# Kernel tuning notes

Measured on AMD Instinct MI355X. Metric: run time of the kernel, lower is better.

Reference implementation:

```python
import jax, jax.numpy as jnp
import numpy as np

N_NODES = 100000
N_EDGES = 1600000
D = 128
HID = 256  # min(2*D, 256)
D_OUT = 128
BN_EPS = 1e-5


def setup_inputs() -> dict:
    key = jax.random.key(0)
    ks = jax.random.split(key, 16)
    s = 0.05
    inp = {
        "x": jax.random.normal(ks[0], (N_NODES, D), dtype=jnp.float32),
        "edges": jax.random.randint(ks[1], (2, N_EDGES), 0, N_NODES, dtype=jnp.int32),
        # affine_before_rnn: Linear(D, D)
        "W_aff": jax.random.normal(ks[2], (D, D), dtype=jnp.float32) * s,
        "b_aff": jnp.zeros((D,), dtype=jnp.float32),
        # GRUCell(D, D)
        "W_ih": jax.random.normal(ks[3], (3 * D, D), dtype=jnp.float32) * s,
        "b_ih": jnp.zeros((3 * D,), dtype=jnp.float32),
        "W_hh": jax.random.normal(ks[4], (3 * D, D), dtype=jnp.float32) * s,
        "b_hh": jnp.zeros((3 * D,), dtype=jnp.float32),
        # merge_layer: Linear(2*D, D)
        "W_merge": jax.random.normal(ks[5], (D, 2 * D), dtype=jnp.float32) * s,
        "b_merge": jnp.zeros((D,), dtype=jnp.float32),
        # learnable self-connection weight
        "eps": jnp.asarray(1.0, dtype=jnp.float32),
        # backbone: Linear(D, HID) -> relu -> Linear(HID, D_OUT) -> relu -> BatchNorm1d
        "W1": jax.random.normal(ks[6], (HID, D), dtype=jnp.float32) * s,
        "b1": jnp.zeros((HID,), dtype=jnp.float32),
        "W2": jax.random.normal(ks[7], (D_OUT, HID), dtype=jnp.float32) * s,
        "b2": jnp.zeros((D_OUT,), dtype=jnp.float32),
        "gamma": jnp.ones((D_OUT,), dtype=jnp.float32),
        "beta": jnp.zeros((D_OUT,), dtype=jnp.float32),
    }
    return inp


def reference(x, edges, W_aff, b_aff, W_ih, b_ih, W_hh, b_hh,
              W_merge, b_merge, eps, W1, b1, W2, b2, gamma, beta):
    src, dst = edges[0], edges[1]
    n = x.shape[0]

    # ---- aggregation 1: 'sum' -> scatter-sum of neighbor features ----
    agg_sum = jax.ops.segment_sum(x[src], dst, num_segments=n)  # (N, D)

    # ---- aggregation 2: 'rnn-max' -> affine, scatter-max, GRUCell ----
    xi = x @ W_aff.T + b_aff
    agg_max = jax.ops.segment_max(xi[src], dst, num_segments=n)  # (N, D)
    agg_max = jnp.where(jnp.isfinite(agg_max), agg_max, 0.0)  # empty segments -> 0

    # GRUCell: input = aggregated neighbors, hidden = original node features
    gi = agg_max @ W_ih.T + b_ih  # (N, 3D)
    gh = x @ W_hh.T + b_hh        # (N, 3D)
    ir, iz, inn = jnp.split(gi, 3, axis=1)
    hr, hz, hn = jnp.split(gh, 3, axis=1)
    r = jax.nn.sigmoid(ir + hr)
    z = jax.nn.sigmoid(iz + hz)
    ncand = jnp.tanh(inn + r * hn)
    rnn_out = (1.0 - z) * ncand + z * x  # (N, D)

    # ---- merge ('cat') ----
    h = jnp.concatenate([agg_sum, rnn_out], axis=1) @ W_merge.T + b_merge  # (N, D)

    # ---- learnable self-connection ----
    h = h + eps * x

    # ---- backbone: dense -> relu -> dense -> relu -> batchnorm1d (train mode) ----
    h = jax.nn.relu(h @ W1.T + b1)
    h = jax.nn.relu(h @ W2.T + b2)
    mean = jnp.mean(h, axis=0)
    var = jnp.mean(jnp.square(h - mean), axis=0)  # biased batch variance
    out = gamma * (h - mean) * jax.lax.rsqrt(var + BN_EPS) + beta
    return out
```

## Files before the change

### kernel.cpp

```cpp
#include <hip/hip_runtime.h>
#include <hip/hip_bf16.h>
#include <math.h>

using bf16 = __hip_bfloat16;
typedef __attribute__((ext_vector_type(8))) short bf16x8;
typedef __attribute__((ext_vector_type(4))) float f32x4;

__device__ __forceinline__ float b2f(unsigned short u) {
  return __uint_as_float(((unsigned)u) << 16);
}
__device__ __forceinline__ unsigned short f2b(float f) {
  bf16 h = __float2bfloat16(f);
  return *reinterpret_cast<unsigned short*>(&h);
}
__device__ __forceinline__ ushort4 f2b4(float4 v) {
  return make_ushort4(f2b(v.x), f2b(v.y), f2b(v.z), f2b(v.w));
}

__global__ __launch_bounds__(256) void mgemm_k(
    const unsigned short* __restrict__ A, int lda, const float* __restrict__ W,
    const float* __restrict__ bias, unsigned short* __restrict__ Cb, int ldc,
    int N, int M, int K) {
  constexpr int LDA = 72;
  __shared__ unsigned short As[128 * LDA];
  __shared__ unsigned short Ws[128 * LDA];

  const int tid = threadIdx.x;
  const int lane = tid & 63;
  const int wave = tid >> 6;
  const int row0 = blockIdx.y * 128;
  const int m0 = blockIdx.x * 128;
  const int rowhalf = (wave & 1) * 64;
  const int colhalf = (wave >> 1) * 64;
  const int l15 = lane & 15;
  const int quad = lane >> 4;

  f32x4 acc[4][4] = {};

  for (int kc = 0; kc < K; kc += 64) {
#pragma unroll
    for (int i = 0; i < 4; i++) {
      int idx = tid + i * 256;
      int r = idx >> 3;
      int k8 = (idx & 7) * 8;
      int row = row0 + r;
      ushort4 u0 = make_ushort4(0, 0, 0, 0), u1 = u0;
      if (row < N) {
        const unsigned short* s = A + (size_t)row * lda + kc + k8;
        u0 = *(const ushort4*)s;
        u1 = *(const ushort4*)(s + 4);
      }
      *(ushort4*)&As[r * LDA + k8] = u0;
      *(ushort4*)&As[r * LDA + k8 + 4] = u1;
    }
#pragma unroll
    for (int i = 0; i < 8; i++) {
      int idx = tid + i * 256;
      int r = idx >> 4;
      int k4 = idx & 15;
      float4 v = *(const float4*)(W + (size_t)(m0 + r) * K + kc + k4 * 4);
      *(ushort4*)&Ws[r * LDA + k4 * 4] = f2b4(v);
    }
    __syncthreads();
#pragma unroll
    for (int ks = 0; ks < 2; ks++) {
      const int ko = ks * 32 + quad * 8;
      bf16x8 af[4], wf[4];
#pragma unroll
      for (int ri = 0; ri < 4; ri++)
        af[ri] = *(const bf16x8*)&As[(rowhalf + ri * 16 + l15) * LDA + ko];
#pragma unroll
      for (int ci = 0; ci < 4; ci++)
        wf[ci] = *(const bf16x8*)&Ws[(colhalf + ci * 16 + l15) * LDA + ko];
#pragma unroll
      for (int ri = 0; ri < 4; ri++)
#pragma unroll
        for (int ci = 0; ci < 4; ci++)
          acc[ri][ci] = __builtin_amdgcn_mfma_f32_16x16x32_bf16(
              af[ri], wf[ci], acc[ri][ci], 0, 0, 0);
    }
    __syncthreads();
  }
#pragma unroll
  for (int ci = 0; ci < 4; ci++) {
    const int col = m0 + colhalf + ci * 16 + l15;
    const float bv = bias[col];
#pragma unroll
    for (int ri = 0; ri < 4; ri++) {
      const int rbase = row0 + rowhalf + ri * 16 + quad * 4;
#pragma unroll
      for (int r = 0; r < 4; r++) {
        int row = rbase + r;
        if (row >= N) continue;
        Cb[(size_t)row * ldc + col] = f2b(acc[ri][ci][r] + bv);
      }
    }
  }
}

__global__ __launch_bounds__(256) void grurnn_k(
    const unsigned short* __restrict__ aggm,
    const unsigned short* __restrict__ xcat,
    const unsigned short* __restrict__ Wbig,
    const float* __restrict__ bias_big, unsigned short* __restrict__ Bcat,
    int N) {
  constexpr int LDA = 72;
  __shared__ unsigned short As[32 * LDA];

  const int tid = threadIdx.x;
  const int lane = tid & 63;
  const int wave = tid >> 6;
  const int l15 = lane & 15;
  const int quad = lane >> 4;
  const int row0 = blockIdx.x * 32;

  f32x4 acc[2][8] = {};

  for (int kc = 0; kc < 256; kc += 64) {
    {
      int r = tid >> 3;
      int k8 = (tid & 7) * 8;
      int row = row0 + r;
      ushort4 u0 = make_ushort4(0, 0, 0, 0), u1 = u0;
      if (row < N) {
        const unsigned short* s =
            (kc < 128) ? aggm + (size_t)row * 128 + kc + k8
                       : xcat + (size_t)row * 256 + (kc - 128) + k8;
        u0 = *(const ushort4*)s;
        u1 = *(const ushort4*)(s + 4);
      }
      *(ushort4*)&As[r * LDA + k8] = u0;
      *(ushort4*)&As[r * LDA + k8 + 4] = u1;
    }
    __syncthreads();
#pragma unroll
    for (int ks = 0; ks < 2; ks++) {
      const int ko = ks * 32 + quad * 8;
      bf16x8 af[2];
#pragma unroll
      for (int ri = 0; ri < 2; ri++)
        af[ri] = *(const bf16x8*)&As[(ri * 16 + l15) * LDA + ko];
#pragma unroll
      for (int ci = 0; ci < 8; ci++) {
        int m = wave * 128 + ci * 16 + l15;
        bf16x8 wf = *(const bf16x8*)&Wbig[(size_t)m * 256 + kc + ko];
#pragma unroll
        for (int ri = 0; ri < 2; ri++)
          acc[ri][ci] = __builtin_amdgcn_mfma_f32_16x16x32_bf16(
              af[ri], wf, acc[ri][ci], 0, 0, 0);
      }
    }
    __syncthreads();
  }
#pragma unroll
  for (int fi = 0; fi < 2; fi++) {
    const int f = wave * 32 + fi * 16 + l15;
    const float br = bias_big[f];
    const float bz = bias_big[128 + f];
    const float bi = bias_big[256 + f];
    const float bh = bias_big[384 + f];
#pragma unroll
    for (int ri = 0; ri < 2; ri++) {
#pragma unroll
      for (int r = 0; r < 4; r++) {
        int row = row0 + ri * 16 + quad * 4 + r;
        if (row >= N) continue;
        float rg = 1.f / (1.f + __expf(-(acc[ri][4 * fi + 0][r] + br)));
        float zg = 1.f / (1.f + __expf(-(acc[ri][4 * fi + 1][r] + bz)));
        float nc =
            tanhf(acc[ri][4 * fi + 2][r] + bi + rg * (acc[ri][4 * fi + 3][r] + bh));
        float xv = b2f(xcat[(size_t)row * 256 + f]);
        Bcat[(size_t)row * 256 + 128 + f] = f2b((1.f - zg) * nc + zg * xv);
      }
    }
  }
}

__global__ __launch_bounds__(256) void backbone_k(
    const unsigned short* __restrict__ Bcat,
    const unsigned short* __restrict__ xcat,
    const unsigned short* __restrict__ Wmb, const float* __restrict__ bm,
    const unsigned short* __restrict__ W1b, const float* __restrict__ b1,
    const unsigned short* __restrict__ W2b, const float* __restrict__ b2,
    const float* __restrict__ epsp, float* __restrict__ out,
    float* __restrict__ stats, int N) {
  constexpr int LDH = 136;
  constexpr int LDH2 = 264;
  __shared__ unsigned short Hp[64 * LDH];
  __shared__ unsigned short Hd[64 * LDH2];
  __shared__ float sbn[128], qbn[128];

  const int tid = threadIdx.x;
  const int lane = tid & 63;
  const int wave = tid >> 6;
  const int l15 = lane & 15;
  const int quad = lane >> 4;
  const int row0 = blockIdx.x * 64;
  if (tid < 128) {
    sbn[tid] = 0.f;
    qbn[tid] = 0.f;
  }
  const float ep = epsp[0];

  {
    f32x4 acc[4][2] = {};
#pragma unroll
    for (int ks = 0; ks < 8; ks++) {
      const int ko = ks * 32 + quad * 8;
      bf16x8 af[4];
#pragma unroll
      for (int ri = 0; ri < 4; ri++)
        af[ri] =
            *(const bf16x8*)&Bcat[(size_t)(row0 + ri * 16 + l15) * 256 + ko];
#pragma unroll
      for (int ci = 0; ci < 2; ci++) {
        bf16x8 wf =
            *(const bf16x8*)&Wmb[(size_t)(wave * 32 + ci * 16 + l15) * 256 + ko];
#pragma unroll
        for (int ri = 0; ri < 4; ri++)
          acc[ri][ci] = __builtin_amdgcn_mfma_f32_16x16x32_bf16(
              af[ri], wf, acc[ri][ci], 0, 0, 0);
      }
    }
#pragma unroll
    for (int ci = 0; ci < 2; ci++) {
      int c = wave * 32 + ci * 16 + l15;
      float bv = bm[c];
#pragma unroll
      for (int ri = 0; ri < 4; ri++) {
#pragma unroll
        for (int r = 0; r < 4; r++) {
          int lr = ri * 16 + quad * 4 + r;
          int row = row0 + lr;
          float v = acc[ri][ci][r] + bv;
          if (row < N) v += ep * b2f(xcat[(size_t)row * 256 + c]);
          Hp[lr * LDH + c] = f2b(v);
        }
      }
    }
  }
  __syncthreads();
  {
    f32x4 acc[4][4] = {};
#pragma unroll
    for (int ks = 0; ks < 4; ks++) {
      const int ko = ks * 32 + quad * 8;
      bf16x8 af[4];
#pragma unroll
      for (int ri = 0; ri < 4; ri++)
        af[ri] = *(const bf16x8*)&Hp[(ri * 16 + l15) * LDH + ko];
#pragma unroll
      for (int ci = 0; ci < 4; ci++) {
        bf16x8 wf =
            *(const bf16x8*)&W1b[(size_t)(wave * 64 + ci * 16 + l15) * 128 + ko];
#pragma unroll
        for (int ri = 0; ri < 4; ri++)
          acc[ri][ci] = __builtin_amdgcn_mfma_f32_16x16x32_bf16(
              af[ri], wf, acc[ri][ci], 0, 0, 0);
      }
    }
    __syncthreads();
#pragma unroll
    for (int ci = 0; ci < 4; ci++) {
      int c = wave * 64 + ci * 16 + l15;
      float bv = b1[c];
#pragma unroll
      for (int ri = 0; ri < 4; ri++) {
#pragma unroll
        for (int r = 0; r < 4; r++) {
          int lr = ri * 16 + quad * 4 + r;
          Hd[lr * LDH2 + c] = f2b(fmaxf(acc[ri][ci][r] + bv, 0.f));
        }
      }
    }
  }
  __syncthreads();
  {
    f32x4 acc[4][2] = {};
#pragma unroll
    for (int ks = 0; ks < 8; ks++) {
      const int ko = ks * 32 + quad * 8;
      bf16x8 af[4];
#pragma unroll
      for (int ri = 0; ri < 4; ri++)
        af[ri] = *(const bf16x8*)&Hd[(ri * 16 + l15) * LDH2 + ko];
#pragma unroll
      for (int ci = 0; ci < 2; ci++) {
        bf16x8 wf =
            *(const bf16x8*)&W2b[(size_t)(wave * 32 + ci * 16 + l15) * 256 + ko];
#pragma unroll
        for (int ri = 0; ri < 4; ri++)
          acc[ri][ci] = __builtin_amdgcn_mfma_f32_16x16x32_bf16(
              af[ri], wf, acc[ri][ci], 0, 0, 0);
      }
    }
#pragma unroll
    for (int ci = 0; ci < 2; ci++) {
      int c = wave * 32 + ci * 16 + l15;
      float bv = b2[c];
      float s = 0.f, q = 0.f;
#pragma unroll
      for (int ri = 0; ri < 4; ri++) {
#pragma unroll
        for (int r = 0; r < 4; r++) {
          int lr = ri * 16 + quad * 4 + r;
          int row = row0 + lr;
          if (row >= N) continue;
          float v = fmaxf(acc[ri][ci][r] + bv, 0.f);
          out[(size_t)row * 128 + c] = v;
          s += v;
          q += v * v;
        }
      }
      atomicAdd(&sbn[c], s);
      atomicAdd(&qbn[c], q);
    }
  }
  __syncthreads();
  if (tid < 128) {
    atomicAdd(&stats[tid], sbn[tid]);
    atomicAdd(&stats[128 + tid], qbn[tid]);
  }
}

__global__ __launch_bounds__(256) void prep_k(
    const float* __restrict__ W_ih, const float* __restrict__ b_ih,
    const float* __restrict__ W_hh, const float* __restrict__ b_hh,
    const float* __restrict__ Wm, const float* __restrict__ W1,
    const float* __restrict__ W2, unsigned short* __restrict__ Wbig,
    unsigned short* __restrict__ Wmb, unsigned short* __restrict__ W1b,
    unsigned short* __restrict__ W2b, float* __restrict__ bias_big,
    float* __restrict__ stats, int* __restrict__ deg, int N) {
  int idx = blockIdx.x * 256 + threadIdx.x;
  if (idx < N) deg[idx] = 0;
  if (idx < 32768) {
    int mp = idx >> 6;
    int k4 = (idx & 63) * 4;
    int w = mp >> 7, ci = (mp >> 4) & 7, l15 = mp & 15;
    int g = ci & 3, fi = ci >> 2;
    int f = w * 32 + fi * 16 + l15;
    const float* src = nullptr;
    int koff = 0;
    if (g <= 1) {
      int m = g * 128 + f;
      if (k4 < 128) { src = W_ih + (size_t)m * 128; koff = k4; }
      else          { src = W_hh + (size_t)m * 128; koff = k4 - 128; }
    } else if (g == 2) {
      if (k4 < 128) { src = W_ih + (size_t)(256 + f) * 128; koff = k4; }
    } else {
      if (k4 >= 128) { src = W_hh + (size_t)(256 + f) * 128; koff = k4 - 128; }
    }
    ushort4 o = make_ushort4(0, 0, 0, 0);
    if (src) o = f2b4(*(const float4*)(src + koff));
    *(ushort4*)&Wbig[(size_t)mp * 256 + k4] = o;
  }
  if (idx < 8192) {
    int m = idx >> 6;
    int k4 = (idx & 63) * 4;
    *(ushort4*)&Wmb[(size_t)m * 256 + k4] =
        f2b4(*(const float4*)(Wm + (size_t)m * 256 + k4));
    *(ushort4*)&W2b[(size_t)m * 256 + k4] =
        f2b4(*(const float4*)(W2 + (size_t)m * 256 + k4));
    int m2 = idx >> 5;
    int k42 = (idx & 31) * 4;
    *(ushort4*)&W1b[(size_t)m2 * 128 + k42] =
        f2b4(*(const float4*)(W1 + (size_t)m2 * 128 + k42));
  }
  if (blockIdx.x == 0) {
    int t = threadIdx.x;
    stats[t] = 0.f;
#pragma unroll
    for (int h = 0; h < 2; h++) {
      int mm = t + h * 256;
      float b;
      if (mm < 256) b = b_ih[mm] + b_hh[mm];
      else if (mm < 384) b = b_ih[mm];
      else b = b_hh[mm - 128];
      bias_big[mm] = b;
    }
  }
}

__global__ __launch_bounds__(256) void cvthist_k(
    const int* __restrict__ edges, int* __restrict__ deg, int E,
    const float* __restrict__ x, unsigned short* __restrict__ xcat,
    int ngroups, int eblk) {
  if ((int)blockIdx.x < eblk) {
    int e = blockIdx.x * 256 + threadIdx.x;
    if (e < E) atomicAdd(&deg[edges[(size_t)E + e]], 1);
  } else {
    int g = (blockIdx.x - eblk) * 256 + threadIdx.x;
    if (g >= ngroups) return;
    int n = g >> 5;
    int j = (g & 31) * 4;
    float4 v = *(const float4*)&x[(size_t)n * 128 + j];
    *(ushort4*)&xcat[(size_t)n * 256 + j] = f2b4(v);
  }
}

__global__ __launch_bounds__(256) void scan1_k(const int* __restrict__ deg,
                                               int* __restrict__ off,
                                               int* __restrict__ bsums, int N) {
  __shared__ int s[256];
  int t = threadIdx.x;
  int i = blockIdx.x * 256 + t;
  int v = (i < N) ? deg[i] : 0;
  s[t] = v;
  __syncthreads();
#pragma unroll
  for (int d = 1; d < 256; d <<= 1) {
    int u = (t >= d) ? s[t - d] : 0;
    __syncthreads();
    s[t] += u;
    __syncthreads();
  }
  if (i < N) off[i] = s[t] - v;
  if (t == 255) bsums[blockIdx.x] = s[255];
}

__global__ __launch_bounds__(512) void scan2_k(int* __restrict__ bsums,
                                               int nb) {
  __shared__ int s[512];
  int t = threadIdx.x;
  int v = (t < nb) ? bsums[t] : 0;
  s[t] = v;
  __syncthreads();
#pragma unroll
  for (int d = 1; d < 512; d <<= 1) {
    int u = (t >= d) ? s[t - d] : 0;
    __syncthreads();
    s[t] += u;
    __syncthreads();
  }
  if (t < nb) bsums[t] = s[t] - v;
}

__global__ __launch_bounds__(256) void scan3_k(int* __restrict__ off,
                                               const int* __restrict__ bsums,
                                               int* __restrict__ binoff,
                                               int* __restrict__ bincur,
                                               int N, int E, int NB) {
  int i = blockIdx.x * 256 + threadIdx.x;
  if (i < N) {
    int o = off[i] + bsums[blockIdx.x];
    off[i] = o;
    if ((i & 511) == 0) {
      binoff[i >> 9] = o;
      bincur[i >> 9] = o;
    }
  }
  if (i == 0) {
    off[N] = E;
    binoff[NB] = E;
  }
}

__global__ __launch_bounds__(256) void edgepart_k(const int* __restrict__ edges,
                                                  int* __restrict__ bincur,
                                                  int* __restrict__ part,
                                                  int E, int NB) {
  __shared__ int cnt[256];
  const int tid = threadIdx.x;
  if (tid < NB) cnt[tid] = 0;
  __syncthreads();
  int sv[16], dv[16];
  const int e0 = blockIdx.x * 4096;
#pragma unroll
  for (int i = 0; i < 16; i++) {
    int e = e0 + i * 256 + tid;
    int s = 0, d = -1;
    if (e < E) {
      s = edges[e];
      d = edges[(size_t)E + e];
    }
    sv[i] = s;
    dv[i] = d;
    if (d >= 0) atomicAdd(&cnt[d >> 9], 1);
  }
  __syncthreads();
  if (tid < NB) {
    int c = cnt[tid];
    int base = c ? atomicAdd(&bincur[tid], c) : 0;
    cnt[tid] = base;
  }
  __syncthreads();
#pragma unroll
  for (int i = 0; i < 16; i++) {
    int d = dv[i];
    if (d < 0) continue;
    int p = atomicAdd(&cnt[d >> 9], 1);
    part[p] = (sv[i] << 9) | (d & 511);
  }
}

__global__ __launch_bounds__(1024) void fill2_k(const int* __restrict__ off,
                                                const int* __restrict__ binoff,
                                                const int* __restrict__ part,
                                                int* __restrict__ bucket,
                                                int N) {
  __shared__ int scur[512];
  const int b = blockIdx.x;
  const int n0 = b << 9;
  const int tid = threadIdx.x;
  if (tid < 512) {
    int node = n0 + tid;
    scur[tid] = (node < N) ? off[node] : 0;
  }
  __syncthreads();
  const int j0 = binoff[b];
  const int j1 = binoff[b + 1];
  for (int j = j0 + tid; j < j1; j += 1024) {
    int p = part[j];
    int pos = atomicAdd(&scur[p & 511], 1);
    bucket[pos] = p >> 9;
  }
}

__global__ __launch_bounds__(256) void gather_k(
    const int* __restrict__ off, const int* __restrict__ bucket,
    const unsigned short* __restrict__ xcat, unsigned short* __restrict__ aggm,
    unsigned short* __restrict__ Bcat, int N) {
  int node = blockIdx.x * 4 + (threadIdx.x >> 6);
  if (node >= N) return;
  const int lane = threadIdx.x & 63;
  const int half = lane >> 5;
  const int f = (lane & 31) * 4;
  const int j0 = off[node], jend = off[node + 1];
  float s0 = 0.f, s1 = 0.f, s2 = 0.f, s3 = 0.f;
  float m0 = -INFINITY, m1 = -INFINITY, m2 = -INFINITY, m3 = -INFINITY;
  int jj = j0 + half;
  int p0 = (jj < jend) ? bucket[jj] : 0;
  int p1 = (jj + 2 < jend) ? bucket[jj + 2] : 0;
  for (; jj < jend; jj += 2) {
    int src = p0;
    p0 = p1;
    p1 = (jj + 4 < jend) ? bucket[jj + 4] : 0;
    ushort4 a = *(const ushort4*)(xcat + (size_t)src * 256 + f);
    ushort4 b = *(const ushort4*)(xcat + (size_t)src * 256 + 128 + f);
    s0 += b2f(a.x);
    s1 += b2f(a.y);
    s2 += b2f(a.z);
    s3 += b2f(a.w);
    m0 = fmaxf(m0, b2f(b.x));
    m1 = fmaxf(m1, b2f(b.y));
    m2 = fmaxf(m2, b2f(b.z));
    m3 = fmaxf(m3, b2f(b.w));
  }
  s0 += __shfl_xor(s0, 32);
  s1 += __shfl_xor(s1, 32);
  s2 += __shfl_xor(s2, 32);
  s3 += __shfl_xor(s3, 32);
  m0 = fmaxf(m0, __shfl_xor(m0, 32));
  m1 = fmaxf(m1, __shfl_xor(m1, 32));
  m2 = fmaxf(m2, __shfl_xor(m2, 32));
  m3 = fmaxf(m3, __shfl_xor(m3, 32));
  if (half == 0) {
    bool nz = jend > j0;
    ushort4 mv = nz ? make_ushort4(f2b(m0), f2b(m1), f2b(m2), f2b(m3))
                    : make_ushort4(0, 0, 0, 0);
    *(ushort4*)&aggm[(size_t)node * 128 + f] = mv;
    *(ushort4*)&Bcat[(size_t)node * 256 + f] =
        make_ushort4(f2b(s0), f2b(s1), f2b(s2), f2b(s3));
  }
}

__global__ __launch_bounds__(256) void bn_apply_k(
    float* __restrict__ out, const float* __restrict__ stats,
    const float* __restrict__ gamma, const float* __restrict__ beta,
    float invn, int nd4) {
  int g = blockIdx.x * 256 + threadIdx.x;
  if (g >= nd4) return;
  int d = (g & 31) * 4;
  float4 v = ((float4*)out)[g];
  float o[4] = {v.x, v.y, v.z, v.w};
#pragma unroll
  for (int i = 0; i < 4; i++) {
    float mean = stats[d + i] * invn;
    float var = fmaxf(stats[128 + d + i] * invn - mean * mean, 0.f);
    float sc = gamma[d + i] * rsqrtf(var + 1e-5f);
    o[i] = (o[i] - mean) * sc + beta[d + i];
  }
  ((float4*)out)[g] = make_float4(o[0], o[1], o[2], o[3]);
}

extern "C" void kernel_launch(void* const* d_in, const int* in_sizes, int n_in,
                              void* d_out, int out_size, void* d_ws,
                              size_t ws_size, hipStream_t stream) {
  (void)n_in;
  (void)out_size;
  (void)ws_size;
  const float* x = (const float*)d_in[0];
  const int* edges = (const int*)d_in[1];
  const float* W_aff = (const float*)d_in[2];
  const float* b_aff = (const float*)d_in[3];
  const float* W_ih = (const float*)d_in[4];
  const float* b_ih = (const float*)d_in[5];
  const float* W_hh = (const float*)d_in[6];
  const float* b_hh = (const float*)d_in[7];
  const float* W_merge = (const float*)d_in[8];
  const float* b_merge = (const float*)d_in[9];
  const float* epsp = (const float*)d_in[10];
  const float* W1 = (const float*)d_in[11];
  const float* b1 = (const float*)d_in[12];
  const float* W2 = (const float*)d_in[13];
  const float* b2 = (const float*)d_in[14];
  const float* gamma = (const float*)d_in[15];
  const float* beta = (const float*)d_in[16];

  const int N = in_sizes[0] / 128;
  const int E = in_sizes[1] / 2;
  const size_t nd = (size_t)N * 128;
  const int NB = (N + 511) >> 9;

  char* base = (char*)d_ws;
  unsigned short* xcat = (unsigned short*)base;
  unsigned short* Bcat = (unsigned short*)(base + (size_t)N * 512);
  unsigned short* aggm = (unsigned short*)(base + (size_t)N * 1024);
  unsigned short* Wbig = (unsigned short*)(base + (size_t)N * 1280);
  unsigned short* Wmb = Wbig + 512 * 256;
  unsigned short* W1b = Wmb + 128 * 256;
  unsigned short* W2b = W1b + 256 * 128;
  float* bias_big = (float*)(W2b + 128 * 256);
  float* stats = bias_big + 512;
  int* deg = (int*)(stats + 512);
  int* off = deg + N;
  int* binoff = off + N + 1;
  int* bincur = binoff + NB + 1;
  int* bucket = bincur + NB;
  int* bsums = bucket + E;
  float* out = (float*)d_out;
  int* part = (int*)d_out;

  const int ny = (N + 127) / 128;
  const int nblk = (N + 255) / 256;
  const int eblk = (E + 255) / 256;
  const int cvtblk = (int)((nd / 4 + 255) / 256);
  const int pgrid = nblk > 128 ? nblk : 128;
  dim3 blk(256);

  prep_k<<<pgrid, blk, 0, stream>>>(W_ih, b_ih, W_hh, b_hh, W_merge, W1, W2,
                                    Wbig, Wmb, W1b, W2b, bias_big, stats, deg,
                                    N);
  cvthist_k<<<eblk + cvtblk, blk, 0, stream>>>(edges, deg, E, x, xcat,
                                               (int)(nd / 4), eblk);
  scan1_k<<<nblk, blk, 0, stream>>>(deg, off, bsums, N);
  scan2_k<<<1, 512, 0, stream>>>(bsums, nblk);
  scan3_k<<<nblk, blk, 0, stream>>>(off, bsums, binoff, bincur, N, E, NB);
  edgepart_k<<<(E + 4095) / 4096, blk, 0, stream>>>(edges, bincur, part, E, NB);
  fill2_k<<<NB, dim3(1024), 0, stream>>>(off, binoff, part, bucket, N);

  mgemm_k<<<dim3(1, ny), blk, 0, stream>>>(xcat, 256, W_aff, b_aff, xcat + 128,
                                           256, N, 128, 128);
  gather_k<<<(N + 3) / 4, blk, 0, stream>>>(off, bucket, xcat, aggm, Bcat, N);
  grurnn_k<<<(N + 31) / 32, blk, 0, stream>>>(aggm, xcat, Wbig, bias_big,
                                              Bcat, N);
  backbone_k<<<(N + 63) / 64, blk, 0, stream>>>(Bcat, xcat, Wmb, b_merge, W1b,
                                                b1, W2b, b2, epsp, out, stats,
                                                N);
  bn_apply_k<<<(int)((nd / 4 + 255) / 256), blk, 0, stream>>>(
      out, stats, gamma, beta, 1.f / (float)N, (int)(nd / 4));
}
```

Before: 647.5 us.

## Split backbone hidden layer into two halves to cut LDS and registers

The backbone kernel now computes the 256-wide hidden layer in two 128-column halves. Each half is written to a smaller shared buffer and immediately accumulated into the second GEMM. This shrinks the Hd shared-memory tile and the per-thread accumulator array, which is meant to allow more resident blocks per CU. In exchange it adds extra __syncthreads barriers per half and keeps a second accumulator live across the loop.

```diff
diff --git a/kernel.cpp b/kernel.cpp
--- a/kernel.cpp
+++ b/kernel.cpp
@@ -185,9 +185,8 @@
     const float* __restrict__ epsp, float* __restrict__ out,
     float* __restrict__ stats, int N) {
   constexpr int LDH = 136;
-  constexpr int LDH2 = 264;
   __shared__ unsigned short Hp[64 * LDH];
-  __shared__ unsigned short Hd[64 * LDH2];
+  __shared__ unsigned short Hd[64 * LDH];
   __shared__ float sbn[128], qbn[128];
 
   const int tid = threadIdx.x;
@@ -240,8 +239,11 @@
     }
   }
   __syncthreads();
-  {
-    f32x4 acc[4][4] = {};
+
+  f32x4 acc3[4][2] = {};
+#pragma unroll
+  for (int hh = 0; hh < 2; hh++) {
+    f32x4 acc2[4][2] = {};
 #pragma unroll
     for (int ks = 0; ks < 4; ks++) {
       const int ko = ks * 32 + quad * 8;
@@ -250,71 +252,71 @@
       for (int ri = 0; ri < 4; ri++)
         af[ri] = *(const bf16x8*)&Hp[(ri * 16 + l15) * LDH + ko];
 #pragma unroll
-      for (int ci = 0; ci < 4; ci++) {
-        bf16x8 wf =
-            *(const bf16x8*)&W1b[(size_t)(wave * 64 + ci * 16 + l15) * 128 + ko];
+      for (int ci = 0; ci < 2; ci++) {
+        bf16x8 wf = *(const bf16x8*)&W1b[(size_t)(hh * 128 + wave * 32 +
+                                                  ci * 16 + l15) *
+                                             128 +
+                                         ko];
 #pragma unroll
         for (int ri = 0; ri < 4; ri++)
-          acc[ri][ci] = __builtin_amdgcn_mfma_f32_16x16x32_bf16(
-              af[ri], wf, acc[ri][ci], 0, 0, 0);
-      }
-    }
-    __syncthreads();
-#pragma unroll
-    for (int ci = 0; ci < 4; ci++) {
-      int c = wave * 64 + ci * 16 + l15;
-      float bv = b1[c];
+          acc2[ri][ci] = __builtin_amdgcn_mfma_f32_16x16x32_bf16(
+              af[ri], wf, acc2[ri][ci], 0, 0, 0);
+      }
+    }
+    __syncthreads();
+#pragma unroll
+    for (int ci = 0; ci < 2; ci++) {
+      int c = wave * 32 + ci * 16 + l15;
+      float bv = b1[hh * 128 + c];
 #pragma unroll
       for (int ri = 0; ri < 4; ri++) {
 #pragma unroll
         for (int r = 0; r < 4; r++) {
           int lr = ri * 16 + quad * 4 + r;
-          Hd[lr * LDH2 + c] = f2b(fmaxf(acc[ri][ci][r] + bv, 0.f));
+          Hd[lr * LDH + c] = f2b(fmaxf(acc2[ri][ci][r] + bv, 0.f));
         }
       }
     }
-  }
-  __syncthreads();
-  {
-    f32x4 acc[4][2] = {};
-#pragma unroll
-    for (int ks = 0; ks < 8; ks++) {
+    __syncthreads();
+#pragma unroll
+    for (int ks = 0; ks < 4; ks++) {
       const int ko = ks * 32 + quad * 8;
       bf16x8 af[4];
 #pragma unroll
       for (int ri = 0; ri < 4; ri++)
-        af[ri] = *(const bf16x8*)&Hd[(ri * 16 + l15) * LDH2 + ko];
+        af[ri] = *(const bf16x8*)&Hd[(ri * 16 + l15) * LDH + ko];
 #pragma unroll
       for (int ci = 0; ci < 2; ci++) {
-        bf16x8 wf =
-            *(const bf16x8*)&W2b[(size_t)(wave * 32 + ci * 16 + l15) * 256 + ko];
+        bf16x8 wf = *(const bf16x8*)&W2b[(size_t)(wave * 32 + ci * 16 + l15) *
+                                             256 +
+                                         hh * 128 + ko];
 #pragma unroll
         for (int ri = 0; ri < 4; ri++)
-          acc[ri][ci] = __builtin_amdgcn_mfma_f32_16x16x32_bf16(
-              af[ri], wf, acc[ri][ci], 0, 0, 0);
-      }
-    }
-#pragma unroll
-    for (int ci = 0; ci < 2; ci++) {
-      int c = wave * 32 + ci * 16 + l15;
-      float bv = b2[c];
-      float s = 0.f, q = 0.f;
-#pragma unroll
-      for (int ri = 0; ri < 4; ri++) {
-#pragma unroll
-        for (int r = 0; r < 4; r++) {
-          int lr = ri * 16 + quad * 4 + r;
-          int row = row0 + lr;
-          if (row >= N) continue;
-          float v = fmaxf(acc[ri][ci][r] + bv, 0.f);
-          out[(size_t)row * 128 + c] = v;
-          s += v;
-          q += v * v;
-        }
-      }
-      atomicAdd(&sbn[c], s);
-      atomicAdd(&qbn[c], q);
-    }
+          acc3[ri][ci] = __builtin_amdgcn_mfma_f32_16x16x32_bf16(
+              af[ri], wf, acc3[ri][ci], 0, 0, 0);
+      }
+    }
+  }
+#pragma unroll
+  for (int ci = 0; ci < 2; ci++) {
+    int c = wave * 32 + ci * 16 + l15;
+    float bv = b2[c];
+    float s = 0.f, q = 0.f;
+#pragma unroll
+    for (int ri = 0; ri < 4; ri++) {
+#pragma unroll
+      for (int r = 0; r < 4; r++) {
+        int lr = ri * 16 + quad * 4 + r;
+        int row = row0 + lr;
+        if (row >= N) continue;
+        float v = fmaxf(acc3[ri][ci][r] + bv, 0.f);
+        out[(size_t)row * 128 + c] = v;
+        s += v;
+        q += v * v;
+      }
+    }
+    atomicAdd(&sbn[c], s);
+    atomicAdd(&qbn[c], q);
   }
   __syncthreads();
   if (tid < 128) {
```

After: 636.0 us. No clear change (-1.8%).
